# Optimization experiments

Measured on AMD Instinct MI355X. Metric: run time of the kernel, lower is better.

Reference implementation:

```python
import jax, jax.numpy as jnp
import numpy as np

K = 32                      # nsample (neighbors)
NPTS = [4096, 2048, 1024]   # npts // downsample_ratios [1,2,4]
CH = [(6, 64, 64), (134, 128, 128), (262, 256, 256)]  # (c_in_edge, c_mid, c_out) per EdgeConv
OUT_CH = 128
EPS = 1e-5


def setup_inputs():
    key = jax.random.key(0)
    ks = iter(jax.random.split(key, 64))
    d = {"pcd": jax.random.normal(next(ks), (8, 4096, 3), dtype=jnp.float32)}
    for li, (cin, cmid, cout) in enumerate(CH, start=1):
        d[f"W{li}a"] = jax.random.normal(next(ks), (cmid, cin), dtype=jnp.float32) * 0.05
        d[f"b{li}a"] = jax.random.normal(next(ks), (cmid,), dtype=jnp.float32) * 0.01
        d[f"g{li}a"] = jnp.ones((cmid,), dtype=jnp.float32)
        d[f"be{li}a"] = jnp.zeros((cmid,), dtype=jnp.float32)
        d[f"W{li}b"] = jax.random.normal(next(ks), (cout, cmid), dtype=jnp.float32) * 0.05
        d[f"b{li}b"] = jax.random.normal(next(ks), (cout,), dtype=jnp.float32) * 0.01
        d[f"g{li}b"] = jnp.ones((cout,), dtype=jnp.float32)
        d[f"be{li}b"] = jnp.zeros((cout,), dtype=jnp.float32)
    d["fcW"] = jax.random.normal(next(ks), (OUT_CH, CH[-1][2]), dtype=jnp.float32) * 0.05
    d["fcb"] = jnp.zeros((OUT_CH,), dtype=jnp.float32)
    return d


def _knn_idx(q, p, k):
    # q: [B,m,3] queries, p: [B,n,3] points -> [B,m,k] nearest-neighbor indices
    d = (jnp.sum(q * q, -1)[:, :, None] + jnp.sum(p * p, -1)[:, None, :]
         - 2.0 * jnp.einsum('bmd,bnd->bmn', q, p))
    _, idx = jax.lax.top_k(-d, k)
    return idx


def _bn(x, g, b):
    # training-mode BatchNorm2d over [B,C,m,k], biased variance (torch behavior)
    mu = jnp.mean(x, axis=(0, 2, 3), keepdims=True)
    var = jnp.mean((x - mu) ** 2, axis=(0, 2, 3), keepdims=True)
    return (x - mu) * jax.lax.rsqrt(var + EPS) * g[None, :, None, None] + b[None, :, None, None]


def _edge_conv(xyz, feat, npoints, params):
    # xyz: [B,n,3], feat: [B,C,n] or None. Range sampling = first npoints points.
    W1, b1, g1, be1, W2, b2, g2, be2 = params
    new_xyz = xyz[:, :npoints]
    # use_xyz=True: concat features (as [B,n,C]) with xyz
    f = xyz if feat is None else jnp.concatenate([jnp.transpose(feat, (0, 2, 1)), xyz], -1)
    new_f = f[:, :npoints]                       # [B,m,D]
    idx = _knn_idx(new_xyz, xyz, K)              # [B,m,K]
    knn_f = jax.vmap(lambda a, i: a[i])(f, idx)  # [B,m,K,D] gather
    tiled = jnp.broadcast_to(new_f[:, :, None, :], knn_f.shape)
    e = jnp.concatenate([knn_f - tiled, tiled], -1)  # [B,m,K,2D] edge features
    h = jnp.einsum('bmkc,oc->bomk', e, W1) + b1[None, :, None, None]
    h = jax.nn.relu(_bn(h, g1, be1))
    h = jnp.einsum('bcmk,oc->bomk', h, W2) + b2[None, :, None, None]
    h = jax.nn.relu(_bn(h, g2, be2))
    return new_xyz, jnp.max(h, axis=-1)          # max-pool over K -> [B,C,m]


def reference(pcd, W1a, b1a, g1a, be1a, W1b, b1b, g1b, be1b,
              W2a, b2a, g2a, be2a, W2b, b2b, g2b, be2b,
              W3a, b3a, g3a, be3a, W3b, b3b, g3b, be3b, fcW, fcb):
    xyz = pcd[..., :3]
    feat = None  # pcd has only xyz channels
    layer_params = [
        (W1a, b1a, g1a, be1a, W1b, b1b, g1b, be1b),
        (W2a, b2a, g2a, be2a, W2b, b2b, g2b, be2b),
        (W3a, b3a, g3a, be3a, W3b, b3b, g3b, be3b),
    ]
    for npoints, p in zip(NPTS, layer_params):
        xyz, feat = _edge_conv(xyz, feat, npoints, p)
    out_feat = jnp.einsum('bcn,oc->bon', feat, fcW) + fcb[None, :, None]
    # Range sampling: idx chain of aranges composes to arange(NPTS[-1])
    idx = jnp.broadcast_to(jnp.arange(NPTS[-1]), (pcd.shape[0], NPTS[-1]))
    return xyz, out_feat, idx, feat
```

## Files before the change

kernel.cpp:

```cpp
#include <hip/hip_runtime.h>
#include <hip/hip_bf16.h>

#define B8 8
#define KNN 32
typedef unsigned short u16;
typedef unsigned int u32;
typedef unsigned long long u64;

typedef __attribute__((ext_vector_type(8))) _Float16 half8;
typedef __attribute__((ext_vector_type(4))) float f32x4;

static __device__ __forceinline__ u16 f2h_u(float f) {
  _Float16 h = (_Float16)f; u16 u; __builtin_memcpy(&u, &h, 2); return u;
}

static __device__ __forceinline__ u64 enc_key(float d, int id) {
  u32 u = __float_as_uint(d);
  u = (d >= 0.f) ? (u | 0x80000000u) : ~u;
  return ((u64)u << 32) | (u32)id;
}
static __device__ __forceinline__ float dec_val(u64 k) {
  u32 u = (u32)(k >> 32);
  u = (u & 0x80000000u) ? (u & 0x7fffffffu) : ~u;
  return __uint_as_float(u);
}

static __device__ __forceinline__ u64 rank64(u64 mk, int lane, u64* slk, u64* outk, float& tau) {
  slk[lane] = mk;
  int r = 0;
#pragma unroll 16
  for (int j = 0; j < 64; ++j) r += (slk[j] < mk) ? 1 : 0;
  outk[r] = mk;
  u64 res = outk[lane];
  tau = dec_val(outk[31]);
  return res;
}

__global__ __launch_bounds__(256) void knn_kernel(const float* __restrict__ pcd,
                                                  int N, int M, int* __restrict__ idxout) {
  __shared__ float4 pts[1024];
  __shared__ u64 bufk[4][32];
  __shared__ u64 slk[4][64];
  __shared__ u64 outk[4][64];
  const int t = threadIdx.x;
  const int lane = t & 63, w = t >> 6;
  const int b = blockIdx.y;
  const int m = blockIdx.x * 4 + w;
  const float* base = pcd + (size_t)b * 4096 * 3;
  const float qx = base[m*3], qy = base[m*3+1], qz = base[m*3+2];
  const float ax = -2.f*qx, ay = -2.f*qy, az = -2.f*qz;

  u64 heldk; float tau; int cnt = 0;

  for (int i = t; i < 1024; i += 256) {
    const float* p = base + (size_t)i * 3;
    float x = p[0], y = p[1], z = p[2];
    pts[i] = make_float4(x, y, z, x*x + y*y + z*z);
  }
  __syncthreads();

  {
    float4 p = pts[lane];
    float r0 = fmaf(ax, p.x, fmaf(ay, p.y, fmaf(az, p.z, p.w)));
    heldk = rank64(enc_key(r0, lane), lane, slk[w], outk[w], tau);
  }

  for (int n0 = 0; n0 < N; n0 += 1024) {
    if (n0) {
      __syncthreads();
      for (int i = t; i < 1024; i += 256) {
        const float* p = base + (size_t)(n0 + i) * 3;
        float x = p[0], y = p[1], z = p[2];
        pts[i] = make_float4(x, y, z, x*x + y*y + z*z);
      }
      __syncthreads();
    }
    for (int c = 0; c < 1024; c += 256) {
      float4 p0 = pts[c + lane];
      float4 p1 = pts[c + 64 + lane];
      float4 p2 = pts[c + 128 + lane];
      float4 p3 = pts[c + 192 + lane];
      float r[4];
      r[0] = fmaf(ax, p0.x, fmaf(ay, p0.y, fmaf(az, p0.z, p0.w)));
      r[1] = fmaf(ax, p1.x, fmaf(ay, p1.y, fmaf(az, p1.z, p1.w)));
      r[2] = fmaf(ax, p2.x, fmaf(ay, p2.y, fmaf(az, p2.z, p2.w)));
      r[3] = fmaf(ax, p3.x, fmaf(ay, p3.y, fmaf(az, p3.z, p3.w)));
      if (n0 == 0 && c == 0) r[0] = 3.4e38f;
      float rmn = fminf(fminf(r[0], r[1]), fminf(r[2], r[3]));
      if (!__any(rmn < tau)) continue;
#pragma unroll
      for (int j = 0; j < 4; ++j) {
        float rr = r[j];
        if (!__any(rr < tau)) continue;
        int gid = n0 + c + j * 64 + lane;
        bool pass = rr < tau;
        while (__any(pass)) {
          u64 mk_ = __ballot(pass);
          int before = __popcll(mk_ & ((1ull << lane) - 1ull));
          int total  = __popcll(mk_);
          int room = 32 - cnt;
          if (pass && before < room) {
            bufk[w][cnt + before] = enc_key(rr, gid);
            pass = false;
          }
          if (total >= room) {
            u64 mk = (lane < 32) ? heldk : bufk[w][lane - 32];
            heldk = rank64(mk, lane, slk[w], outk[w], tau);
            cnt = 0;
            pass = pass && (rr < tau);
          } else {
            cnt += total;
          }
        }
      }
    }
  }
  if (cnt > 0) {
    int bl = lane - 32;
    u64 mk = (lane < 32) ? heldk
             : ((bl < cnt) ? bufk[w][bl]
                           : ((0xFFFFFFFFull << 32) | (0xFFFFFF00u | (u32)lane)));
    heldk = rank64(mk, lane, slk[w], outk[w], tau);
  }
  if (lane < KNN) idxout[((size_t)b * M + m) * KNN + lane] = (int)(u32)(heldk & 0xFFFFFFFFu);
}

__global__ void prep_all(
    const float* __restrict__ W1a, const float* __restrict__ W1b,
    const float* __restrict__ W2a, const float* __restrict__ W2b,
    const float* __restrict__ W3a, const float* __restrict__ W3b,
    float* __restrict__ RED,
    float* __restrict__ WAT1, float* __restrict__ WBT1, u16* __restrict__ WBH1,
    float* __restrict__ WBT2, u16* __restrict__ WAH2, u16* __restrict__ WBH2,
    float* __restrict__ WBT3, u16* __restrict__ WAH3, u16* __restrict__ WBH3)
{
  int i0 = blockIdx.x * 256 + threadIdx.x;
  int NT = gridDim.x * 256;
  for (int i = i0; i < 8192; i += NT) RED[i] = 0.f;
  for (int i = i0; i < 256; i += NT) {
    int c = i >> 6, o = i & 63;
    float w1 = (c < 3) ? W1a[o*6 + c] : 0.f;
    float w2 = (c < 3) ? W1a[o*6 + 3 + c] : 0.f;
    WAT1[i] = w1; WBT1[i] = w2 - w1;
  }
  for (int i = i0; i < 4096; i += NT) WBH1[i] = f2h_u(W1b[i]);
  for (int i = i0; i < 68*128; i += NT) {
    int c = i >> 7, o = i & 127;
    float w1 = 0.f, w2 = 0.f;
    if (c < 67) { w1 = W2a[o*134 + c]; w2 = W2a[o*134 + 67 + c]; }
    WBT2[i] = w2 - w1;
  }
  for (int i = i0; i < 128*128; i += NT) {
    int o = i >> 7, k = i & 127;
    WAH2[i] = (k < 67) ? f2h_u(W2a[o*134 + k]) : (u16)0;
  }
  for (int i = i0; i < 16384; i += NT) WBH2[i] = f2h_u(W2b[i]);
  for (int i = i0; i < 132*256; i += NT) {
    int c = i >> 8, o = i & 255;
    float w1 = 0.f, w2 = 0.f;
    if (c < 131) { w1 = W3a[o*262 + c]; w2 = W3a[o*262 + 131 + c]; }
    WBT3[i] = w2 - w1;
  }
  for (int i = i0; i < 256*192; i += NT) {
    int o = i / 192, k = i - o * 192;
    WAH3[i] = (k < 131) ? f2h_u(W3a[o*262 + k]) : (u16)0;
  }
  for (int i = i0; i < 65536; i += NT) WBH3[i] = f2h_u(W3b[i]);
}

template<int C2, int CM, int MODE>
__global__ __launch_bounds__(256) void conv_a_gemm(
    const float* __restrict__ F, size_t fbstride,
    const int* __restrict__ idx,
    const float* __restrict__ Wt,
    const float* __restrict__ bias,
    const float* __restrict__ T,
    float* __restrict__ Tout,
    float* __restrict__ red_s, float* __restrict__ red_q,
    int M)
{
  constexpr int KP = (C2 + 3) & ~3;
  constexpr int KC = (KP <= 68) ? KP : 44;
  __shared__ float At[64][KC];
  __shared__ float Wts[KC][64];
  __shared__ int ji[64];
  __shared__ float sred[4][64];
  __shared__ float qred[4][64];
  const int t = threadIdx.x;
  const int rt = blockIdx.x, ot = blockIdx.y, b = blockIdx.z;
  const int R0 = rt * 64, oc0 = ot * 64;
  const float* Fb = F + (size_t)b * fbstride;

  if (t < 64) {
    int gr = R0 + t;
    ji[t] = (MODE == 0) ? gr : idx[((size_t)b * M + (gr >> 5)) * KNN + (gr & 31)];
  }

  const int cg = t & 15, rg = t >> 4;
  const int r0 = rg * 4, c0 = cg * 4;
  float acc[4][4];
  if (MODE == 0) {
#pragma unroll
    for (int j = 0; j < 4; ++j) {
      float bv = bias[oc0 + c0 + j];
#pragma unroll
      for (int i = 0; i < 4; ++i) acc[i][j] = bv;
    }
  } else {
#pragma unroll
    for (int i = 0; i < 4; ++i) {
      const float* tp = T + ((size_t)b * M + (size_t)((R0 + r0 + i) >> 5)) * CM + oc0 + c0;
      acc[i][0] = tp[0]; acc[i][1] = tp[1]; acc[i][2] = tp[2]; acc[i][3] = tp[3];
    }
  }
  __syncthreads();

  for (int k0 = 0; k0 < KP; k0 += KC) {
    if (k0) __syncthreads();
    for (int i = t; i < KC * 64; i += 256) {
      int c = i >> 6, o = i & 63;
      Wts[c][o] = Wt[(size_t)(k0 + c) * CM + oc0 + o];
    }
    if constexpr (C2 == 3) {
      for (int i = t; i < 64 * 4; i += 256) {
        int r = i >> 2, c = i & 3;
        At[r][c] = (c < 3) ? Fb[(size_t)ji[r] * 3 + c] : 0.f;
      }
    } else {
      constexpr int C4 = KC / 4;
      for (int i = t; i < 64 * C4; i += 256) {
        int r = i / C4, c4 = i - r * C4;
        *(float4*)&At[r][c4 * 4] = *(const float4*)&Fb[(size_t)ji[r] * KP + k0 + c4 * 4];
      }
    }
    __syncthreads();

#pragma unroll 4
    for (int k = 0; k < KC; ++k) {
      const float4 w4 = *(const float4*)&Wts[k][c0];
      float a0 = At[r0][k], a1 = At[r0+1][k], a2 = At[r0+2][k], a3 = At[r0+3][k];
      acc[0][0]=fmaf(a0,w4.x,acc[0][0]); acc[0][1]=fmaf(a0,w4.y,acc[0][1]);
      acc[0][2]=fmaf(a0,w4.z,acc[0][2]); acc[0][3]=fmaf(a0,w4.w,acc[0][3]);
      acc[1][0]=fmaf(a1,w4.x,acc[1][0]); acc[1][1]=fmaf(a1,w4.y,acc[1][1]);
      acc[1][2]=fmaf(a1,w4.z,acc[1][2]); acc[1][3]=fmaf(a1,w4.w,acc[1][3]);
      acc[2][0]=fmaf(a2,w4.x,acc[2][0]); acc[2][1]=fmaf(a2,w4.y,acc[2][1]);
      acc[2][2]=fmaf(a2,w4.z,acc[2][2]); acc[2][3]=fmaf(a2,w4.w,acc[2][3]);
      acc[3][0]=fmaf(a3,w4.x,acc[3][0]); acc[3][1]=fmaf(a3,w4.y,acc[3][1]);
      acc[3][2]=fmaf(a3,w4.z,acc[3][2]); acc[3][3]=fmaf(a3,w4.w,acc[3][3]);
    }
  }

  if (MODE == 0) {
    float* op = Tout + ((size_t)b * M + R0) * (size_t)CM + oc0;
#pragma unroll
    for (int i = 0; i < 4; ++i) {
      float* p = op + (size_t)(r0 + i) * CM + c0;
      p[0]=acc[i][0]; p[1]=acc[i][1]; p[2]=acc[i][2]; p[3]=acc[i][3];
    }
  } else {
    float cs[4], cq_[4];
#pragma unroll
    for (int j = 0; j < 4; ++j) {
      float s = acc[0][j] + acc[1][j] + acc[2][j] + acc[3][j];
      float q = acc[0][j]*acc[0][j] + acc[1][j]*acc[1][j] + acc[2][j]*acc[2][j] + acc[3][j]*acc[3][j];
      s += __shfl_xor(s, 16); q += __shfl_xor(q, 16);
      s += __shfl_xor(s, 32); q += __shfl_xor(q, 32);
      cs[j] = s; cq_[j] = q;
    }
    const int wv = t >> 6;
    if ((t & 48) == 0) {
#pragma unroll
      for (int j = 0; j < 4; ++j) { sred[wv][c0 + j] = cs[j]; qred[wv][c0 + j] = cq_[j]; }
    }
    __syncthreads();
    if (t < 64) {
      float s = sred[0][t] + sred[1][t] + sred[2][t] + sred[3][t];
      float q = qred[0][t] + qred[1][t] + qred[2][t] + qred[3][t];
      int shdw = (rt & 15) * 256;
      atomicAdd(&red_s[shdw + t], s);
      atomicAdd(&red_q[shdw + t], q);
    }
  }
}

__global__ __launch_bounds__(256) void l1_convb(
    const float* __restrict__ pcd,
    const int* __restrict__ idx,
    const float* __restrict__ WAT,
    const float* __restrict__ T,
    const u16* __restrict__ Wbh,
    const float* __restrict__ bb,
    const float* __restrict__ sc1, const float* __restrict__ sh1,
    float* __restrict__ red_s, float* __restrict__ red_q,
    float* __restrict__ hmax)
{
  __shared__ u16 Alds[64][72];
  __shared__ u16 Wlds[64][72];
  __shared__ float xyzs[64][4];
  __shared__ float was[3][64];
  __shared__ float scs[64], shs[64];
  __shared__ int ji[64];
  const int t = threadIdx.x;
  const int lane = t & 63, w = t >> 6;
  const int wr = w >> 1, wc = w & 1;
  const int cl = lane & 15, rq = lane >> 4;
  const int rt = blockIdx.x, b = blockIdx.y;
  const int R0 = rt * 64;
  const float* pb = pcd + (size_t)b * 12288;

  if (t < 64) ji[t] = idx[((size_t)b * 4096 + ((R0 + t) >> 5)) * KNN + ((R0 + t) & 31)];
  if (t < 192) was[t / 64][t & 63] = WAT[t];
  for (int i = t; i < 64 * 8; i += 256) {
    int o = i >> 3, seg = i & 7;
    *(float4*)&Wlds[o][seg * 8] = *(const float4*)&Wbh[(size_t)o * 64 + seg * 8];
  }
  __syncthreads();
  if (t < 64) {
    const float* p = pb + (size_t)ji[t] * 3;
    xyzs[t][0] = p[0]; xyzs[t][1] = p[1]; xyzs[t][2] = p[2]; xyzs[t][3] = 0.f;
  }
  if (t < 64) { scs[t] = sc1[t]; shs[t] = sh1[t]; }
  __syncthreads();

  for (int i = t; i < 64 * 8; i += 256) {
    int r = i >> 3, seg = i & 7;
    float px = xyzs[r][0], py = xyzs[r][1], pz = xyzs[r][2];
    const float* Tm = T + ((size_t)b * 4096 + (size_t)((R0 + r) >> 5)) * 64;
    half8 ov;
#pragma unroll
    for (int j2 = 0; j2 < 8; ++j2) {
      int c = seg * 8 + j2;
      float h = Tm[c];
      h = fmaf(px, was[0][c], h);
      h = fmaf(py, was[1][c], h);
      h = fmaf(pz, was[2][c], h);
      ov[j2] = (_Float16)fmaxf(0.f, fmaf(h, scs[c], shs[c]));
    }
    *(half8*)&Alds[r][seg * 8] = ov;
  }
  __syncthreads();

  f32x4 acc[2][2];
#pragma unroll
  for (int fr = 0; fr < 2; ++fr)
#pragma unroll
    for (int fc = 0; fc < 2; ++fc) {
      float bv = bb[wc * 32 + fc * 16 + cl];
#pragma unroll
      for (int r = 0; r < 4; ++r) acc[fr][fc][r] = bv;
    }

#pragma unroll
  for (int kk = 0; kk < 2; ++kk) {
    half8 af[2], bf[2];
#pragma unroll
    for (int fr = 0; fr < 2; ++fr)
      af[fr] = *(const half8*)&Alds[wr*32 + fr*16 + cl][kk*32 + rq*8];
#pragma unroll
    for (int fc = 0; fc < 2; ++fc)
      bf[fc] = *(const half8*)&Wlds[wc*32 + fc*16 + cl][kk*32 + rq*8];
#pragma unroll
    for (int fr = 0; fr < 2; ++fr)
#pragma unroll
      for (int fc = 0; fc < 2; ++fc)
        acc[fr][fc] = __builtin_amdgcn_mfma_f32_16x16x32_f16(af[fr], bf[fc], acc[fr][fc], 0, 0, 0);
  }

#pragma unroll
  for (int fc = 0; fc < 2; ++fc) {
    float s = 0.f, q = 0.f, mx = -3.4e38f;
#pragma unroll
    for (int fr = 0; fr < 2; ++fr)
#pragma unroll
      for (int r = 0; r < 4; ++r) {
        float v = acc[fr][fc][r];
        s += v; q += v * v; mx = fmaxf(mx, v);
      }
    s += __shfl_xor(s, 16); q += __shfl_xor(q, 16); mx = fmaxf(mx, __shfl_xor(mx, 16));
    s += __shfl_xor(s, 32); q += __shfl_xor(q, 32); mx = fmaxf(mx, __shfl_xor(mx, 32));
    if (rq == 0) {
      int col = wc * 32 + fc * 16 + cl;
      int shdw = (rt & 15) * 256;
      atomicAdd(&red_s[shdw + col], s);
      atomicAdd(&red_q[shdw + col], q);
      hmax[((size_t)b * 4096 + (size_t)(rt * 2 + wr)) * 64 + col] = mx;
    }
  }
}

template<int CM, int KPAD>
__global__ __launch_bounds__(256) void conv_a_mfma(
    const float* __restrict__ F, int fstride, size_t fbstride,
    const int* __restrict__ idx,
    const u16* __restrict__ Wh,
    const float* __restrict__ T,
    u32* __restrict__ H32,
    float* __restrict__ red_s, float* __restrict__ red_q,
    int M)
{
  constexpr int FC = CM / 32;
  __shared__ u16 Alds[64][72];
  __shared__ u16 Wlds[CM][72];
  __shared__ int ji[64];
  const int t = threadIdx.x;
  const int lane = t & 63, w = t >> 6;
  const int wr = w >> 1, wc = w & 1;
  const int cl = lane & 15, rq = lane >> 4;
  const int rt = blockIdx.x, b = blockIdx.y;
  const int R0 = rt * 64;
  const float* Fb = F + (size_t)b * fbstride;

  if (t < 64) ji[t] = idx[((size_t)b * M + ((R0 + t) >> 5)) * KNN + ((R0 + t) & 31)];

  f32x4 acc[2][FC];
#pragma unroll
  for (int fr = 0; fr < 2; ++fr)
#pragma unroll
    for (int fc = 0; fc < FC; ++fc) {
      int col = wc * (CM/2) + fc * 16 + cl;
#pragma unroll
      for (int r = 0; r < 4; ++r) {
        int row = R0 + wr*32 + fr*16 + rq*4 + r;
        acc[fr][fc][r] = T[((size_t)b * M + (row >> 5)) * CM + col];
      }
    }
  __syncthreads();

  for (int k0 = 0; k0 < KPAD; k0 += 64) {
    if (k0) __syncthreads();
    for (int i = t; i < 64 * 16; i += 256) {
      int r = i >> 4, seg = i & 15;
      int k = k0 + seg * 4;
      ushort4 s = {0,0,0,0};
      if (k < fstride) {
        float4 v = *(const float4*)&Fb[(size_t)ji[r] * fstride + k];
        s.x = f2h_u(v.x); s.y = f2h_u(v.y); s.z = f2h_u(v.z); s.w = f2h_u(v.w);
      }
      *(ushort4*)&Alds[r][seg * 4] = s;
    }
    for (int i = t; i < CM * 8; i += 256) {
      int o = i >> 3, seg = i & 7;
      *(float4*)&Wlds[o][seg * 8] = *(const float4*)&Wh[(size_t)o * KPAD + k0 + seg * 8];
    }
    __syncthreads();

#pragma unroll
    for (int kk = 0; kk < 2; ++kk) {
      half8 af[2], bf[FC];
#pragma unroll
      for (int fr = 0; fr < 2; ++fr)
        af[fr] = *(const half8*)&Alds[wr*32 + fr*16 + cl][kk*32 + rq*8];
#pragma unroll
      for (int fc = 0; fc < FC; ++fc)
        bf[fc] = *(const half8*)&Wlds[wc*(CM/2) + fc*16 + cl][kk*32 + rq*8];
#pragma unroll
      for (int fr = 0; fr < 2; ++fr)
#pragma unroll
        for (int fc = 0; fc < FC; ++fc)
          acc[fr][fc] = __builtin_amdgcn_mfma_f32_16x16x32_f16(af[fr], bf[fc], acc[fr][fc], 0, 0, 0);
    }
  }

  u32* Hb4 = H32 + ((size_t)b * ((size_t)M * KNN / 4) + (size_t)(R0 >> 2)) * CM;
#pragma unroll
  for (int fr = 0; fr < 2; ++fr)
#pragma unroll
    for (int fc = 0; fc < FC; ++fc) {
      int col = wc*(CM/2) + fc*16 + cl;
      u32 v = __builtin_amdgcn_cvt_pk_fp8_f32(acc[fr][fc][0], acc[fr][fc][1], 0, false);
      v = __builtin_amdgcn_cvt_pk_fp8_f32(acc[fr][fc][2], acc[fr][fc][3], v, true);
      Hb4[(size_t)(wr*8 + fr*4 + rq) * CM + col] = v;
    }

#pragma unroll
  for (int fc = 0; fc < FC; ++fc) {
    float s = 0.f, q = 0.f;
#pragma unroll
    for (int fr = 0; fr < 2; ++fr)
#pragma unroll
      for (int r = 0; r < 4; ++r) {
        float v = acc[fr][fc][r];
        s += v; q += v * v;
      }
    s += __shfl_xor(s, 16); q += __shfl_xor(q, 16);
    s += __shfl_xor(s, 32); q += __shfl_xor(q, 32);
    if (rq == 0) {
      int col = wc*(CM/2) + fc*16 + cl;
      int shdw = (rt & 15) * 256;
      atomicAdd(&red_s[shdw + col], s);
      atomicAdd(&red_q[shdw + col], q);
    }
  }
}

template<int CM>
__global__ __launch_bounds__(512) void conv_b_fused(
    const u32* __restrict__ H32,
    const u16* __restrict__ Wh,
    const float* __restrict__ bb,
    const float* __restrict__ sc1, const float* __restrict__ sh1,
    float* __restrict__ red_s, float* __restrict__ red_q,
    float* __restrict__ hmax,
    int Mrows)
{
  constexpr int FC = CM / 32;
  __shared__ u16 Alds[128][72];
  __shared__ u16 Wlds[CM][72];
  __shared__ float scs[CM], shs[CM];
  const int t = threadIdx.x;
  const int lane = t & 63, w = t >> 6;
  const int wr = w >> 1;
  const int wc = w & 1;
  const int cl = lane & 15, rq = lane >> 4;
  const int rt = blockIdx.x, b = blockIdx.y;
  const u32* Hb4 = H32 + ((size_t)b * ((size_t)Mrows / 4) + (size_t)(rt * 32)) * CM;

  for (int i = t; i < CM; i += 512) { scs[i] = sc1[i]; shs[i] = sh1[i]; }

  f32x4 acc[2][FC];
#pragma unroll
  for (int fr = 0; fr < 2; ++fr)
#pragma unroll
    for (int fc = 0; fc < FC; ++fc) {
      float bv = bb[wc * (CM/2) + fc * 16 + cl];
#pragma unroll
      for (int r = 0; r < 4; ++r) acc[fr][fc][r] = bv;
    }
  __syncthreads();

  for (int k0 = 0; k0 < CM; k0 += 64) {
    if (k0) __syncthreads();
    for (int i = t; i < 128 * 8; i += 512) {
      int r = i >> 3, seg = i & 7;
      int rg = r >> 2, sh8 = (r & 3) * 8;
      const u32* hp = Hb4 + (size_t)rg * CM + k0 + seg * 8;
      half8 ov;
#pragma unroll
      for (int j = 0; j < 8; ++j) {
        float v = __builtin_amdgcn_cvt_f32_fp8((hp[j] >> sh8) & 0xffu, 0);
        int c = k0 + seg * 8 + j;
        v = fmaxf(0.f, fmaf(v, scs[c], shs[c]));
        ov[j] = (_Float16)v;
      }
      *(half8*)&Alds[r][seg * 8] = ov;
    }
    for (int i = t; i < CM * 8; i += 512) {
      int o = i >> 3, seg = i & 7;
      *(float4*)&Wlds[o][seg * 8] = *(const float4*)&Wh[(size_t)o * CM + k0 + seg * 8];
    }
    __syncthreads();

#pragma unroll
    for (int kk = 0; kk < 2; ++kk) {
      half8 af[2], bf[FC];
#pragma unroll
      for (int fr = 0; fr < 2; ++fr)
        af[fr] = *(const half8*)&Alds[wr*32 + fr*16 + cl][kk*32 + rq*8];
#pragma unroll
      for (int fc = 0; fc < FC; ++fc)
        bf[fc] = *(const half8*)&Wlds[wc*(CM/2) + fc*16 + cl][kk*32 + rq*8];
#pragma unroll
      for (int fr = 0; fr < 2; ++fr)
#pragma unroll
        for (int fc = 0; fc < FC; ++fc)
          acc[fr][fc] = __builtin_amdgcn_mfma_f32_16x16x32_f16(af[fr], bf[fc], acc[fr][fc], 0, 0, 0);
    }
  }

#pragma unroll
  for (int fc = 0; fc < FC; ++fc) {
    float s = 0.f, q = 0.f, mx = -3.4e38f;
#pragma unroll
    for (int fr = 0; fr < 2; ++fr)
#pragma unroll
      for (int r = 0; r < 4; ++r) {
        float v = acc[fr][fc][r];
        s += v; q += v * v; mx = fmaxf(mx, v);
      }
    s += __shfl_xor(s, 16); q += __shfl_xor(q, 16); mx = fmaxf(mx, __shfl_xor(mx, 16));
    s += __shfl_xor(s, 32); q += __shfl_xor(q, 32); mx = fmaxf(mx, __shfl_xor(mx, 32));
    if (rq == 0) {
      int col = wc*(CM/2) + fc*16 + cl;
      int shdw = (rt & 15) * 256;
      atomicAdd(&red_s[shdw + col], s);
      atomicAdd(&red_q[shdw + col], q);
      hmax[((size_t)b * (Mrows >> 5) + (size_t)(rt * 4 + wr)) * CM + col] = mx;
    }
  }
}

__global__ void bn_finalize(float* __restrict__ red_s, float* __restrict__ red_q,
                            const float* __restrict__ g, const float* __restrict__ be,
                            float* __restrict__ sc, float* __restrict__ sh,
                            int cm, float invcnt) {
  int o = threadIdx.x;
  if (o < cm) {
    float s = 0.f, q = 0.f;
    for (int i = 0; i < 16; ++i) { s += red_s[i * 256 + o]; q += red_q[i * 256 + o]; }
    float mu  = s * invcnt;
    float var = fmaxf(q * invcnt - mu * mu, 0.f);
    float scv = g[o] * rsqrtf(var + 1e-5f);
    sc[o] = scv;
    sh[o] = fmaf(-mu, scv, be[o]);
  }
  __syncthreads();
  for (int i = threadIdx.x; i < 16 * 256; i += 256) { red_s[i] = 0.f; red_q[i] = 0.f; }
}

__global__ __launch_bounds__(256) void bnrelu_fb(const float* __restrict__ hm,
    const float* __restrict__ sc2, const float* __restrict__ sh2,
    float* __restrict__ fout, int CM, int fostride, size_t fobstride, int M) {
  int i = blockIdx.x * 256 + threadIdx.x;
  int cq = CM >> 2;
  int total = B8 * M * cq;
  if (i >= total) return;
  int c4 = i % cq; int r = i / cq;
  int b = r / M, m = r - b * M;
  float4 v = *(const float4*)&hm[((size_t)b * M + m) * CM + c4 * 4];
  int c = c4 * 4;
  float4 o;
  o.x = fmaxf(0.f, fmaf(v.x, sc2[c],   sh2[c]));
  o.y = fmaxf(0.f, fmaf(v.y, sc2[c+1], sh2[c+1]));
  o.z = fmaxf(0.f, fmaf(v.z, sc2[c+2], sh2[c+2]));
  o.w = fmaxf(0.f, fmaf(v.w, sc2[c+3], sh2[c+3]));
  *(float4*)&fout[(size_t)b * fobstride + (size_t)m * fostride + c] = o;
}

__global__ void append_xyz(const float* __restrict__ pcd, float* __restrict__ fbuf,
                           int nrows, int stride, int coff) {
  int i = blockIdx.x * 256 + threadIdx.x;
  if (i < B8 * nrows) {
    int b = i / nrows, n = i - b * nrows;
    const float* p = pcd + ((size_t)b * 4096 + n) * 3;
    float* dd = fbuf + ((size_t)b * nrows + n) * stride + coff;
    dd[0] = p[0]; dd[1] = p[1]; dd[2] = p[2]; dd[3] = 0.f;
  }
}

__global__ __launch_bounds__(256) void fc_out(const float* __restrict__ f4,
                                              const float* __restrict__ fcW, const float* __restrict__ fcb,
                                              float* __restrict__ out1, float* __restrict__ out3) {
  __shared__ float tile[32 * 257];
  const int t = threadIdx.x, b = blockIdx.x, n0 = blockIdx.y * 32;
  for (int i = t; i < 32 * 256; i += 256) {
    int n = i >> 8, c = i & 255;
    tile[n * 257 + c] = f4[((size_t)b * 1024 + n0 + n) * 256 + c];
  }
  __syncthreads();
  const int n = t & 31, og = t >> 5;
#pragma unroll
  for (int ci = 0; ci < 32; ++ci) {
    int c = og * 32 + ci;
    out3[((size_t)b * 256 + c) * 1024 + n0 + n] = tile[n * 257 + c];
  }
#pragma unroll
  for (int oi = 0; oi < 16; ++oi) {
    int o = og * 16 + oi;
    float acc = fcb[o];
    const float* w = fcW + (size_t)o * 256;
#pragma unroll 4
    for (int c = 0; c < 256; ++c) acc = fmaf(tile[n * 257 + c], w[c], acc);
    out1[((size_t)b * 128 + o) * 1024 + n0 + n] = acc;
  }
}

__global__ void out_xyz_idx(const float* __restrict__ pcd, float* __restrict__ out0,
                            float* __restrict__ out2) {
  int i = blockIdx.x * 256 + threadIdx.x;
  if (i < B8 * 1024) {
    int b = i >> 10, n = i & 1023;
    const float* p = pcd + ((size_t)b * 4096 + n) * 3;
    float* o = out0 + (size_t)i * 3;
    o[0] = p[0]; o[1] = p[1]; o[2] = p[2];
    out2[i] = (float)n;
  }
}

extern "C" void kernel_launch(void* const* d_in, const int* in_sizes, int n_in,
                              void* d_out, int out_size, void* d_ws, size_t ws_size,
                              hipStream_t stream) {
  (void)in_sizes; (void)n_in; (void)out_size; (void)ws_size;
  const float* pcd = (const float*)d_in[0];
  const float* W1a = (const float*)d_in[1];  const float* b1a = (const float*)d_in[2];
  const float* g1a = (const float*)d_in[3];  const float* be1a= (const float*)d_in[4];
  const float* W1b = (const float*)d_in[5];  const float* b1b = (const float*)d_in[6];
  const float* g1b = (const float*)d_in[7];  const float* be1b= (const float*)d_in[8];
  const float* W2a = (const float*)d_in[9];  const float* b2a = (const float*)d_in[10];
  const float* g2a = (const float*)d_in[11]; const float* be2a= (const float*)d_in[12];
  const float* W2b = (const float*)d_in[13]; const float* b2b = (const float*)d_in[14];
  const float* g2b = (const float*)d_in[15]; const float* be2b= (const float*)d_in[16];
  const float* W3a = (const float*)d_in[17]; const float* b3a = (const float*)d_in[18];
  const float* g3a = (const float*)d_in[19]; const float* be3a= (const float*)d_in[20];
  const float* W3b = (const float*)d_in[21]; const float* b3b = (const float*)d_in[22];
  const float* g3b = (const float*)d_in[23]; const float* be3b= (const float*)d_in[24];
  const float* fcW = (const float*)d_in[25]; const float* fcb = (const float*)d_in[26];

  float* wsf = (float*)d_ws;
  float* FB2 = wsf;
  float* FB3 = FB2 + 2228224;
  float* FB4 = FB3 + 2162688;
  float* TBUF= FB4 + 2097152;
  float* RED = TBUF + 2097152;
  float* red_s = RED, *red_q = RED + 4096;
  float* SC1 = RED + 8192;  float* SH1 = SC1 + 256;
  float* SC2 = SH1 + 256;   float* SH2 = SC2 + 256;
  float* WAT1 = SH2 + 256;
  float* WBT1 = WAT1 + 256;
  float* WBT2 = WBT1 + 256;
  float* WBT3 = WBT2 + 8704;
  float* HMAX = WBT3 + 33792;
  int* IDX1 = (int*)(HMAX + 2097152);
  int* IDX2 = IDX1 + (size_t)8 * 4096 * 32;
  int* IDX3 = IDX2 + (size_t)8 * 2048 * 32;
  u32* H32  = (u32*)(IDX3 + (size_t)8 * 1024 * 32);
  u16* WBH1 = (u16*)(H32 + 16777216);
  u16* WAH2 = WBH1 + 4096;
  u16* WBH2 = WAH2 + 16384;
  u16* WAH3 = WBH2 + 16384;
  u16* WBH3 = WAH3 + 49152;

  float* out0 = (float*)d_out;
  float* out1 = out0 + 24576;
  float* out2 = out1 + 1048576;
  float* out3 = out2 + 8192;

  prep_all<<<64, 256, 0, stream>>>(W1a, W1b, W2a, W2b, W3a, W3b, RED,
                                   WAT1, WBT1, WBH1, WBT2, WAH2, WBH2, WBT3, WAH3, WBH3);

  knn_kernel<<<dim3(1024, 8), 256, 0, stream>>>(pcd, 4096, 4096, IDX1);
  conv_a_gemm<3,64,0><<<dim3(64,1,8),256,0,stream>>>(pcd,(size_t)12288,nullptr,WBT1,b1a,nullptr,TBUF,nullptr,nullptr,4096);
  conv_a_gemm<3,64,1><<<dim3(2048,1,8),256,0,stream>>>(pcd,(size_t)12288,IDX1,WAT1,nullptr,TBUF,nullptr,red_s,red_q,4096);
  bn_finalize<<<1,256,0,stream>>>(red_s,red_q,g1a,be1a,SC1,SH1,64,1.f/1048576.f);
  l1_convb<<<dim3(2048,8),256,0,stream>>>(pcd,IDX1,WAT1,TBUF,WBH1,b1b,SC1,SH1,red_s,red_q,HMAX);
  bn_finalize<<<1,256,0,stream>>>(red_s,red_q,g1b,be1b,SC2,SH2,64,1.f/1048576.f);
  bnrelu_fb<<<2048,256,0,stream>>>(HMAX,SC2,SH2,FB2,64,68,(size_t)278528,4096);
  append_xyz<<<128, 256, 0, stream>>>(pcd, FB2, 4096, 68, 64);

  knn_kernel<<<dim3(512, 8), 256, 0, stream>>>(pcd, 4096, 2048, IDX2);
  conv_a_gemm<67,128,0><<<dim3(32,2,8),256,0,stream>>>(FB2,(size_t)278528,nullptr,WBT2,b2a,nullptr,TBUF,nullptr,nullptr,2048);
  conv_a_mfma<128,128><<<dim3(1024,8),256,0,stream>>>(FB2,68,(size_t)278528,IDX2,WAH2,TBUF,H32,red_s,red_q,2048);
  bn_finalize<<<1,256,0,stream>>>(red_s,red_q,g2a,be2a,SC1,SH1,128,1.f/524288.f);
  conv_b_fused<128><<<dim3(512,8),512,0,stream>>>(H32,WBH2,b2b,SC1,SH1,red_s,red_q,HMAX,2048*32);
  bn_finalize<<<1,256,0,stream>>>(red_s,red_q,g2b,be2b,SC2,SH2,128,1.f/524288.f);
  bnrelu_fb<<<2048,256,0,stream>>>(HMAX,SC2,SH2,FB3,128,132,(size_t)270336,2048);
  append_xyz<<<64, 256, 0, stream>>>(pcd, FB3, 2048, 132, 128);

  knn_kernel<<<dim3(256, 8), 256, 0, stream>>>(pcd, 2048, 1024, IDX3);
  conv_a_gemm<131,256,0><<<dim3(16,4,8),256,0,stream>>>(FB3,(size_t)270336,nullptr,WBT3,b3a,nullptr,TBUF,nullptr,nullptr,1024);
  conv_a_mfma<256,192><<<dim3(512,8),256,0,stream>>>(FB3,132,(size_t)270336,IDX3,WAH3,TBUF,H32,red_s,red_q,1024);
  bn_finalize<<<1,256,0,stream>>>(red_s,red_q,g3a,be3a,SC1,SH1,256,1.f/262144.f);
  conv_b_fused<256><<<dim3(256,8),512,0,stream>>>(H32,WBH3,b3b,SC1,SH1,red_s,red_q,HMAX,1024*32);
  bn_finalize<<<1,256,0,stream>>>(red_s,red_q,g3b,be3b,SC2,SH2,256,1.f/262144.f);
  bnrelu_fb<<<2048,256,0,stream>>>(HMAX,SC2,SH2,FB4,256,256,(size_t)262144,1024);

  fc_out<<<dim3(8, 32), 256, 0, stream>>>(FB4, fcW, fcb, out1, out3);
  out_xyz_idx<<<32, 256, 0, stream>>>(pcd, out0, out2);
}
```

Before: 849.7 us.

## Reuse layer-1 kNN indices for layer 2 and vectorize kNN point loads

Layer 2 queries the first 2048 points against the same 4096-point cloud that layer 1 already searched, so its neighbor lists are identical to the first rows of IDX1. The second kNN launch is removed, and conv_a_mfma gains an index-stride parameter so it can read IDX1 directly. Separately, the kNN kernel now stages points into shared memory with three float4 loads per thread instead of scalar strided loads. The reuse depends on layer-2 sampling being exactly the first points of the same xyz set.

```diff
diff --git a/kernel.cpp b/kernel.cpp
--- a/kernel.cpp
+++ b/kernel.cpp
@@ -52,10 +52,13 @@
 
   u64 heldk; float tau; int cnt = 0;
 
-  for (int i = t; i < 1024; i += 256) {
-    const float* p = base + (size_t)i * 3;
-    float x = p[0], y = p[1], z = p[2];
-    pts[i] = make_float4(x, y, z, x*x + y*y + z*z);
+  {
+    const float4* src = (const float4*)(base) + (size_t)t * 3;
+    float4 va = src[0], vb = src[1], vc = src[2];
+    pts[t*4+0] = make_float4(va.x, va.y, va.z, fmaf(va.x,va.x, fmaf(va.y,va.y, va.z*va.z)));
+    pts[t*4+1] = make_float4(va.w, vb.x, vb.y, fmaf(va.w,va.w, fmaf(vb.x,vb.x, vb.y*vb.y)));
+    pts[t*4+2] = make_float4(vb.z, vb.w, vc.x, fmaf(vb.z,vb.z, fmaf(vb.w,vb.w, vc.x*vc.x)));
+    pts[t*4+3] = make_float4(vc.y, vc.z, vc.w, fmaf(vc.y,vc.y, fmaf(vc.z,vc.z, vc.w*vc.w)));
   }
   __syncthreads();
 
@@ -68,11 +71,12 @@
   for (int n0 = 0; n0 < N; n0 += 1024) {
     if (n0) {
       __syncthreads();
-      for (int i = t; i < 1024; i += 256) {
-        const float* p = base + (size_t)(n0 + i) * 3;
-        float x = p[0], y = p[1], z = p[2];
-        pts[i] = make_float4(x, y, z, x*x + y*y + z*z);
-      }
+      const float4* src = (const float4*)(base + (size_t)n0 * 3) + (size_t)t * 3;
+      float4 va = src[0], vb = src[1], vc = src[2];
+      pts[t*4+0] = make_float4(va.x, va.y, va.z, fmaf(va.x,va.x, fmaf(va.y,va.y, va.z*va.z)));
+      pts[t*4+1] = make_float4(va.w, vb.x, vb.y, fmaf(va.w,va.w, fmaf(vb.x,vb.x, vb.y*vb.y)));
+      pts[t*4+2] = make_float4(vb.z, vb.w, vc.x, fmaf(vb.z,vb.z, fmaf(vb.w,vb.w, vc.x*vc.x)));
+      pts[t*4+3] = make_float4(vc.y, vc.z, vc.w, fmaf(vc.y,vc.y, fmaf(vc.z,vc.z, vc.w*vc.w)));
       __syncthreads();
     }
     for (int c = 0; c < 1024; c += 256) {
@@ -391,7 +395,7 @@
 template<int CM, int KPAD>
 __global__ __launch_bounds__(256) void conv_a_mfma(
     const float* __restrict__ F, int fstride, size_t fbstride,
-    const int* __restrict__ idx,
+    const int* __restrict__ idx, int idxstride,
     const u16* __restrict__ Wh,
     const float* __restrict__ T,
     u32* __restrict__ H32,
@@ -410,7 +414,7 @@
   const int R0 = rt * 64;
   const float* Fb = F + (size_t)b * fbstride;
 
-  if (t < 64) ji[t] = idx[((size_t)b * M + ((R0 + t) >> 5)) * KNN + ((R0 + t) & 31)];
+  if (t < 64) ji[t] = idx[((size_t)b * idxstride + ((R0 + t) >> 5)) * KNN + ((R0 + t) & 31)];
 
   f32x4 acc[2][FC];
 #pragma unroll
@@ -710,8 +714,7 @@
   float* WBT3 = WBT2 + 8704;
   float* HMAX = WBT3 + 33792;
   int* IDX1 = (int*)(HMAX + 2097152);
-  int* IDX2 = IDX1 + (size_t)8 * 4096 * 32;
-  int* IDX3 = IDX2 + (size_t)8 * 2048 * 32;
+  int* IDX3 = IDX1 + (size_t)8 * 4096 * 32;
   u32* H32  = (u32*)(IDX3 + (size_t)8 * 1024 * 32);
   u16* WBH1 = (u16*)(H32 + 16777216);
   u16* WAH2 = WBH1 + 4096;
@@ -736,9 +739,8 @@
   bnrelu_fb<<<2048,256,0,stream>>>(HMAX,SC2,SH2,FB2,64,68,(size_t)278528,4096);
   append_xyz<<<128, 256, 0, stream>>>(pcd, FB2, 4096, 68, 64);
 
-  knn_kernel<<<dim3(512, 8), 256, 0, stream>>>(pcd, 4096, 2048, IDX2);
   conv_a_gemm<67,128,0><<<dim3(32,2,8),256,0,stream>>>(FB2,(size_t)278528,nullptr,WBT2,b2a,nullptr,TBUF,nullptr,nullptr,2048);
-  conv_a_mfma<128,128><<<dim3(1024,8),256,0,stream>>>(FB2,68,(size_t)278528,IDX2,WAH2,TBUF,H32,red_s,red_q,2048);
+  conv_a_mfma<128,128><<<dim3(1024,8),256,0,stream>>>(FB2,68,(size_t)278528,IDX1,4096,WAH2,TBUF,H32,red_s,red_q,2048);
   bn_finalize<<<1,256,0,stream>>>(red_s,red_q,g2a,be2a,SC1,SH1,128,1.f/524288.f);
   conv_b_fused<128><<<dim3(512,8),512,0,stream>>>(H32,WBH2,b2b,SC1,SH1,red_s,red_q,HMAX,2048*32);
   bn_finalize<<<1,256,0,stream>>>(red_s,red_q,g2b,be2b,SC2,SH2,128,1.f/524288.f);
@@ -747,7 +749,7 @@
 
   knn_kernel<<<dim3(256, 8), 256, 0, stream>>>(pcd, 2048, 1024, IDX3);
   conv_a_gemm<131,256,0><<<dim3(16,4,8),256,0,stream>>>(FB3,(size_t)270336,nullptr,WBT3,b3a,nullptr,TBUF,nullptr,nullptr,1024);
-  conv_a_mfma<256,192><<<dim3(512,8),256,0,stream>>>(FB3,132,(size_t)270336,IDX3,WAH3,TBUF,H32,red_s,red_q,1024);
+  conv_a_mfma<256,192><<<dim3(512,8),256,0,stream>>>(FB3,132,(size_t)270336,IDX3,1024,WAH3,TBUF,H32,red_s,red_q,1024);
   bn_finalize<<<1,256,0,stream>>>(red_s,red_q,g3a,be3a,SC1,SH1,256,1.f/262144.f);
   conv_b_fused<256><<<dim3(256,8),512,0,stream>>>(H32,WBH3,b3b,SC1,SH1,red_s,red_q,HMAX,1024*32);
   bn_finalize<<<1,256,0,stream>>>(red_s,red_q,g3b,be3b,SC2,SH2,256,1.f/262144.f);
```

After: 774.1 us. 8.9% less time.

## Split KNN queries across wave pairs, fuse BN finalize, reuse layer-1 KNN

Applied to the files above, without the earlier changes.

The KNN kernel now gives each query two wavefronts, each scanning half of the point tile and sharing their pruning threshold, then merges the two partial top-32 lists. This doubles the grid to raise parallelism on the dominant KNN stage. The separate bn_finalize launches are removed: each consumer kernel computes scale and shift from per-layer reduction buffers, which are zeroed once in prep. The append_xyz kernel is folded into bnrelu_fb. Layer 2 reuses IDX1, because the first 2048 points' neighbours among all 4096 points are the same as layer 1's, so the second KNN launch is dropped. The cost is some redundant per-block BN arithmetic and extra sync and merge work in KNN.

```diff
diff --git a/kernel.cpp b/kernel.cpp
--- a/kernel.cpp
+++ b/kernel.cpp
@@ -36,17 +36,33 @@
   return res;
 }
 
+static __device__ __forceinline__ void bn_from_red(int o, const float* red_s, const float* red_q,
+                                                   const float* g, const float* be, float invcnt,
+                                                   float* scs, float* shs) {
+  float s = 0.f, q = 0.f;
+#pragma unroll
+  for (int i = 0; i < 16; ++i) { s += red_s[i * 256 + o]; q += red_q[i * 256 + o]; }
+  float mu  = s * invcnt;
+  float var = fmaxf(q * invcnt - mu * mu, 0.f);
+  float scv = g[o] * rsqrtf(var + 1e-5f);
+  scs[o] = scv;
+  shs[o] = fmaf(-mu, scv, be[o]);
+}
+
 __global__ __launch_bounds__(256) void knn_kernel(const float* __restrict__ pcd,
                                                   int N, int M, int* __restrict__ idxout) {
   __shared__ float4 pts[1024];
   __shared__ u64 bufk[4][32];
   __shared__ u64 slk[4][64];
   __shared__ u64 outk[4][64];
+  __shared__ float taus[4];
+  __shared__ u64 mergek[2][32];
   const int t = threadIdx.x;
   const int lane = t & 63, w = t >> 6;
+  const int q = w >> 1, h = w & 1;
   const int b = blockIdx.y;
-  const int m = blockIdx.x * 4 + w;
-  const float* base = pcd + (size_t)b * 4096 * 3;
+  const int m = blockIdx.x * 2 + q;
+  const float* base = pcd + (size_t)b * 12288;
   const float qx = base[m*3], qy = base[m*3+1], qz = base[m*3+2];
   const float ax = -2.f*qx, ay = -2.f*qy, az = -2.f*qz;
 
@@ -60,13 +76,14 @@
   __syncthreads();
 
   {
-    float4 p = pts[lane];
+    float4 p = pts[h * 512 + lane];
     float r0 = fmaf(ax, p.x, fmaf(ay, p.y, fmaf(az, p.z, p.w)));
-    heldk = rank64(enc_key(r0, lane), lane, slk[w], outk[w], tau);
+    heldk = rank64(enc_key(r0, h * 512 + lane), lane, slk[w], outk[w], tau);
   }
 
   for (int n0 = 0; n0 < N; n0 += 1024) {
     if (n0) {
+      taus[w] = tau;
       __syncthreads();
       for (int i = t; i < 1024; i += 256) {
         const float* p = base + (size_t)(n0 + i) * 3;
@@ -74,8 +91,10 @@
         pts[i] = make_float4(x, y, z, x*x + y*y + z*z);
       }
       __syncthreads();
-    }
-    for (int c = 0; c < 1024; c += 256) {
+      tau = fminf(tau, taus[w ^ 1]);
+    }
+    for (int cc = 0; cc < 512; cc += 256) {
+      const int c = h * 512 + cc;
       float4 p0 = pts[c + lane];
       float4 p1 = pts[c + 64 + lane];
       float4 p2 = pts[c + 128 + lane];
@@ -85,7 +104,7 @@
       r[1] = fmaf(ax, p1.x, fmaf(ay, p1.y, fmaf(az, p1.z, p1.w)));
       r[2] = fmaf(ax, p2.x, fmaf(ay, p2.y, fmaf(az, p2.z, p2.w)));
       r[3] = fmaf(ax, p3.x, fmaf(ay, p3.y, fmaf(az, p3.z, p3.w)));
-      if (n0 == 0 && c == 0) r[0] = 3.4e38f;
+      if (n0 == 0 && cc == 0) r[0] = 3.4e38f;
       float rmn = fminf(fminf(r[0], r[1]), fminf(r[2], r[3]));
       if (!__any(rmn < tau)) continue;
 #pragma unroll
@@ -122,7 +141,13 @@
                            : ((0xFFFFFFFFull << 32) | (0xFFFFFF00u | (u32)lane)));
     heldk = rank64(mk, lane, slk[w], outk[w], tau);
   }
-  if (lane < KNN) idxout[((size_t)b * M + m) * KNN + lane] = (int)(u32)(heldk & 0xFFFFFFFFu);
+  if (h == 1 && lane < 32) mergek[q][lane] = heldk;
+  __syncthreads();
+  if (h == 0) {
+    u64 mk = (lane < 32) ? heldk : mergek[q][lane - 32];
+    heldk = rank64(mk, lane, slk[w], outk[w], tau);
+    if (lane < 32) idxout[((size_t)b * M + m) * KNN + lane] = (int)(u32)(heldk & 0xFFFFFFFFu);
+  }
 }
 
 __global__ void prep_all(
@@ -136,7 +161,7 @@
 {
   int i0 = blockIdx.x * 256 + threadIdx.x;
   int NT = gridDim.x * 256;
-  for (int i = i0; i < 8192; i += NT) RED[i] = 0.f;
+  for (int i = i0; i < 49152; i += NT) RED[i] = 0.f;
   for (int i = i0; i < 256; i += NT) {
     int c = i >> 6, o = i & 63;
     float w1 = (c < 3) ? W1a[o*6 + c] : 0.f;
@@ -290,8 +315,9 @@
     const float* __restrict__ T,
     const u16* __restrict__ Wbh,
     const float* __restrict__ bb,
-    const float* __restrict__ sc1, const float* __restrict__ sh1,
-    float* __restrict__ red_s, float* __restrict__ red_q,
+    const float* __restrict__ gA, const float* __restrict__ beA,
+    const float* __restrict__ redA_s, const float* __restrict__ redA_q,
+    float* __restrict__ redB_s, float* __restrict__ redB_q,
     float* __restrict__ hmax)
 {
   __shared__ u16 Alds[64][72];
@@ -310,6 +336,7 @@
 
   if (t < 64) ji[t] = idx[((size_t)b * 4096 + ((R0 + t) >> 5)) * KNN + ((R0 + t) & 31)];
   if (t < 192) was[t / 64][t & 63] = WAT[t];
+  if (t >= 192) bn_from_red(t - 192, redA_s, redA_q, gA, beA, 1.f/1048576.f, scs, shs);
   for (int i = t; i < 64 * 8; i += 256) {
     int o = i >> 3, seg = i & 7;
     *(float4*)&Wlds[o][seg * 8] = *(const float4*)&Wbh[(size_t)o * 64 + seg * 8];
@@ -319,7 +346,6 @@
     const float* p = pb + (size_t)ji[t] * 3;
     xyzs[t][0] = p[0]; xyzs[t][1] = p[1]; xyzs[t][2] = p[2]; xyzs[t][3] = 0.f;
   }
-  if (t < 64) { scs[t] = sc1[t]; shs[t] = sh1[t]; }
   __syncthreads();
 
   for (int i = t; i < 64 * 8; i += 256) {
@@ -330,11 +356,11 @@
 #pragma unroll
     for (int j2 = 0; j2 < 8; ++j2) {
       int c = seg * 8 + j2;
-      float h = Tm[c];
-      h = fmaf(px, was[0][c], h);
-      h = fmaf(py, was[1][c], h);
-      h = fmaf(pz, was[2][c], h);
-      ov[j2] = (_Float16)fmaxf(0.f, fmaf(h, scs[c], shs[c]));
+      float hh = Tm[c];
+      hh = fmaf(px, was[0][c], hh);
+      hh = fmaf(py, was[1][c], hh);
+      hh = fmaf(pz, was[2][c], hh);
+      ov[j2] = (_Float16)fmaxf(0.f, fmaf(hh, scs[c], shs[c]));
     }
     *(half8*)&Alds[r][seg * 8] = ov;
   }
@@ -381,8 +407,8 @@
     if (rq == 0) {
       int col = wc * 32 + fc * 16 + cl;
       int shdw = (rt & 15) * 256;
-      atomicAdd(&red_s[shdw + col], s);
-      atomicAdd(&red_q[shdw + col], q);
+      atomicAdd(&redB_s[shdw + col], s);
+      atomicAdd(&redB_q[shdw + col], q);
       hmax[((size_t)b * 4096 + (size_t)(rt * 2 + wr)) * 64 + col] = mx;
     }
   }
@@ -391,7 +417,7 @@
 template<int CM, int KPAD>
 __global__ __launch_bounds__(256) void conv_a_mfma(
     const float* __restrict__ F, int fstride, size_t fbstride,
-    const int* __restrict__ idx,
+    const int* __restrict__ idx, int idxstride,
     const u16* __restrict__ Wh,
     const float* __restrict__ T,
     u32* __restrict__ H32,
@@ -410,7 +436,7 @@
   const int R0 = rt * 64;
   const float* Fb = F + (size_t)b * fbstride;
 
-  if (t < 64) ji[t] = idx[((size_t)b * M + ((R0 + t) >> 5)) * KNN + ((R0 + t) & 31)];
+  if (t < 64) ji[t] = idx[((size_t)b * idxstride + ((R0 + t) >> 5)) * KNN + ((R0 + t) & 31)];
 
   f32x4 acc[2][FC];
 #pragma unroll
@@ -498,8 +524,9 @@
     const u32* __restrict__ H32,
     const u16* __restrict__ Wh,
     const float* __restrict__ bb,
-    const float* __restrict__ sc1, const float* __restrict__ sh1,
-    float* __restrict__ red_s, float* __restrict__ red_q,
+    const float* __restrict__ gA, const float* __restrict__ beA,
+    const float* __restrict__ redA_s, const float* __restrict__ redA_q, float invcnt,
+    float* __restrict__ redB_s, float* __restrict__ redB_q,
     float* __restrict__ hmax,
     int Mrows)
 {
@@ -515,7 +542,7 @@
   const int rt = blockIdx.x, b = blockIdx.y;
   const u32* Hb4 = H32 + ((size_t)b * ((size_t)Mrows / 4) + (size_t)(rt * 32)) * CM;
 
-  for (int i = t; i < CM; i += 512) { scs[i] = sc1[i]; shs[i] = sh1[i]; }
+  for (int i = t; i < CM; i += 512) bn_from_red(i, redA_s, redA_q, gA, beA, invcnt, scs, shs);
 
   f32x4 acc[2][FC];
 #pragma unroll
@@ -582,34 +609,21 @@
     if (rq == 0) {
       int col = wc*(CM/2) + fc*16 + cl;
       int shdw = (rt & 15) * 256;
-      atomicAdd(&red_s[shdw + col], s);
-      atomicAdd(&red_q[shdw + col], q);
+      atomicAdd(&redB_s[shdw + col], s);
+      atomicAdd(&redB_q[shdw + col], q);
       hmax[((size_t)b * (Mrows >> 5) + (size_t)(rt * 4 + wr)) * CM + col] = mx;
     }
   }
 }
 
-__global__ void bn_finalize(float* __restrict__ red_s, float* __restrict__ red_q,
-                            const float* __restrict__ g, const float* __restrict__ be,
-                            float* __restrict__ sc, float* __restrict__ sh,
-                            int cm, float invcnt) {
-  int o = threadIdx.x;
-  if (o < cm) {
-    float s = 0.f, q = 0.f;
-    for (int i = 0; i < 16; ++i) { s += red_s[i * 256 + o]; q += red_q[i * 256 + o]; }
-    float mu  = s * invcnt;
-    float var = fmaxf(q * invcnt - mu * mu, 0.f);
-    float scv = g[o] * rsqrtf(var + 1e-5f);
-    sc[o] = scv;
-    sh[o] = fmaf(-mu, scv, be[o]);
-  }
-  __syncthreads();
-  for (int i = threadIdx.x; i < 16 * 256; i += 256) { red_s[i] = 0.f; red_q[i] = 0.f; }
-}
-
 __global__ __launch_bounds__(256) void bnrelu_fb(const float* __restrict__ hm,
-    const float* __restrict__ sc2, const float* __restrict__ sh2,
+    const float* __restrict__ gB, const float* __restrict__ beB,
+    const float* __restrict__ redB_s, const float* __restrict__ redB_q, float invcnt,
+    const float* __restrict__ pcd,
     float* __restrict__ fout, int CM, int fostride, size_t fobstride, int M) {
+  __shared__ float scs[256], shs[256];
+  for (int o = threadIdx.x; o < CM; o += 256) bn_from_red(o, redB_s, redB_q, gB, beB, invcnt, scs, shs);
+  __syncthreads();
   int i = blockIdx.x * 256 + threadIdx.x;
   int cq = CM >> 2;
   int total = B8 * M * cq;
@@ -619,21 +633,15 @@
   float4 v = *(const float4*)&hm[((size_t)b * M + m) * CM + c4 * 4];
   int c = c4 * 4;
   float4 o;
-  o.x = fmaxf(0.f, fmaf(v.x, sc2[c],   sh2[c]));
-  o.y = fmaxf(0.f, fmaf(v.y, sc2[c+1], sh2[c+1]));
-  o.z = fmaxf(0.f, fmaf(v.z, sc2[c+2], sh2[c+2]));
-  o.w = fmaxf(0.f, fmaf(v.w, sc2[c+3], sh2[c+3]));
-  *(float4*)&fout[(size_t)b * fobstride + (size_t)m * fostride + c] = o;
-}
-
-__global__ void append_xyz(const float* __restrict__ pcd, float* __restrict__ fbuf,
-                           int nrows, int stride, int coff) {
-  int i = blockIdx.x * 256 + threadIdx.x;
-  if (i < B8 * nrows) {
-    int b = i / nrows, n = i - b * nrows;
-    const float* p = pcd + ((size_t)b * 4096 + n) * 3;
-    float* dd = fbuf + ((size_t)b * nrows + n) * stride + coff;
-    dd[0] = p[0]; dd[1] = p[1]; dd[2] = p[2]; dd[3] = 0.f;
+  o.x = fmaxf(0.f, fmaf(v.x, scs[c],   shs[c]));
+  o.y = fmaxf(0.f, fmaf(v.y, scs[c+1], shs[c+1]));
+  o.z = fmaxf(0.f, fmaf(v.z, scs[c+2], shs[c+2]));
+  o.w = fmaxf(0.f, fmaf(v.w, scs[c+3], shs[c+3]));
+  float* op = fout + (size_t)b * fobstride + (size_t)m * fostride;
+  *(float4*)(op + c) = o;
+  if (pcd && c4 == 0) {
+    const float* p = pcd + ((size_t)b * 4096 + m) * 3;
+    *(float4*)(op + CM) = make_float4(p[0], p[1], p[2], 0.f);
   }
 }
 
@@ -701,17 +709,16 @@
   float* FB4 = FB3 + 2162688;
   float* TBUF= FB4 + 2097152;
   float* RED = TBUF + 2097152;
-  float* red_s = RED, *red_q = RED + 4096;
-  float* SC1 = RED + 8192;  float* SH1 = SC1 + 256;
-  float* SC2 = SH1 + 256;   float* SH2 = SC2 + 256;
-  float* WAT1 = SH2 + 256;
+  float* R1A = RED;          float* R1B = RED + 8192;
+  float* R2A = RED + 16384;  float* R2B = RED + 24576;
+  float* R3A = RED + 32768;  float* R3B = RED + 40960;
+  float* WAT1 = RED + 49152;
   float* WBT1 = WAT1 + 256;
   float* WBT2 = WBT1 + 256;
   float* WBT3 = WBT2 + 8704;
   float* HMAX = WBT3 + 33792;
   int* IDX1 = (int*)(HMAX + 2097152);
-  int* IDX2 = IDX1 + (size_t)8 * 4096 * 32;
-  int* IDX3 = IDX2 + (size_t)8 * 2048 * 32;
+  int* IDX3 = IDX1 + (size_t)8 * 4096 * 32;
   u32* H32  = (u32*)(IDX3 + (size_t)8 * 1024 * 32);
   u16* WBH1 = (u16*)(H32 + 16777216);
   u16* WAH2 = WBH1 + 4096;
@@ -727,31 +734,22 @@
   prep_all<<<64, 256, 0, stream>>>(W1a, W1b, W2a, W2b, W3a, W3b, RED,
                                    WAT1, WBT1, WBH1, WBT2, WAH2, WBH2, WBT3, WAH3, WBH3);
 
-  knn_kernel<<<dim3(1024, 8), 256, 0, stream>>>(pcd, 4096, 4096, IDX1);
+  knn_kernel<<<dim3(2048, 8), 256, 0, stream>>>(pcd, 4096, 4096, IDX1);
   conv_a_gemm<3,64,0><<<dim3(64,1,8),256,0,stream>>>(pcd,(size_t)12288,nullptr,WBT1,b1a,nullptr,TBUF,nullptr,nullptr,4096);
-  conv_a_gemm<3,64,1><<<dim3(2048,1,8),256,0,stream>>>(pcd,(size_t)12288,IDX1,WAT1,nullptr,TBUF,nullptr,red_s,red_q,4096);
-  bn_finalize<<<1,256,0,stream>>>(red_s,red_q,g1a,be1a,SC1,SH1,64,1.f/1048576.f);
-  l1_convb<<<dim3(2048,8),256,0,stream>>>(pcd,IDX1,WAT1,TBUF,WBH1,b1b,SC1,SH1,red_s,red_q,HMAX);
-  bn_finalize<<<1,256,0,stream>>>(red_s,red_q,g1b,be1b,SC2,SH2,64,1.f/1048576.f);
-  bnrelu_fb<<<2048,256,0,stream>>>(HMAX,SC2,SH2,FB2,64,68,(size_t)278528,4096);
-  append_xyz<<<128, 256, 0, stream>>>(pcd, FB2, 4096, 68, 64);
-
-  knn_kernel<<<dim3(512, 8), 256, 0, stream>>>(pcd, 4096, 2048, IDX2);
+  conv_a_gemm<3,64,1><<<dim3(2048,1,8),256,0,stream>>>(pcd,(size_t)12288,IDX1,WAT1,nullptr,TBUF,nullptr,R1A,R1A+4096,4096);
+  l1_convb<<<dim3(2048,8),256,0,stream>>>(pcd,IDX1,WAT1,TBUF,WBH1,b1b,g1a,be1a,R1A,R1A+4096,R1B,R1B+4096,HMAX);
+  bnrelu_fb<<<2048,256,0,stream>>>(HMAX,g1b,be1b,R1B,R1B+4096,1.f/1048576.f,pcd,FB2,64,68,(size_t)278528,4096);
+
   conv_a_gemm<67,128,0><<<dim3(32,2,8),256,0,stream>>>(FB2,(size_t)278528,nullptr,WBT2,b2a,nullptr,TBUF,nullptr,nullptr,2048);
-  conv_a_mfma<128,128><<<dim3(1024,8),256,0,stream>>>(FB2,68,(size_t)278528,IDX2,WAH2,TBUF,H32,red_s,red_q,2048);
-  bn_finalize<<<1,256,0,stream>>>(red_s,red_q,g2a,be2a,SC1,SH1,128,1.f/524288.f);
-  conv_b_fused<128><<<dim3(512,8),512,0,stream>>>(H32,WBH2,b2b,SC1,SH1,red_s,red_q,HMAX,2048*32);
-  bn_finalize<<<1,256,0,stream>>>(red_s,red_q,g2b,be2b,SC2,SH2,128,1.f/524288.f);
-  bnrelu_fb<<<2048,256,0,stream>>>(HMAX,SC2,SH2,FB3,128,132,(size_t)270336,2048);
-  append_xyz<<<64, 256, 0, stream>>>(pcd, FB3, 2048, 132, 128);
-
-  knn_kernel<<<dim3(256, 8), 256, 0, stream>>>(pcd, 2048, 1024, IDX3);
+  conv_a_mfma<128,128><<<dim3(1024,8),256,0,stream>>>(FB2,68,(size_t)278528,IDX1,4096,WAH2,TBUF,H32,R2A,R2A+4096,2048);
+  conv_b_fused<128><<<dim3(512,8),512,0,stream>>>(H32,WBH2,b2b,g2a,be2a,R2A,R2A+4096,1.f/524288.f,R2B,R2B+4096,HMAX,2048*32);
+  bnrelu_fb<<<2048,256,0,stream>>>(HMAX,g2b,be2b,R2B,R2B+4096,1.f/524288.f,pcd,FB3,128,132,(size_t)270336,2048);
+
+  knn_kernel<<<dim3(512, 8), 256, 0, stream>>>(pcd, 2048, 1024, IDX3);
   conv_a_gemm<131,256,0><<<dim3(16,4,8),256,0,stream>>>(FB3,(size_t)270336,nullptr,WBT3,b3a,nullptr,TBUF,nullptr,nullptr,1024);
-  conv_a_mfma<256,192><<<dim3(512,8),256,0,stream>>>(FB3,132,(size_t)270336,IDX3,WAH3,TBUF,H32,red_s,red_q,1024);
-  bn_finalize<<<1,256,0,stream>>>(red_s,red_q,g3a,be3a,SC1,SH1,256,1.f/262144.f);
-  conv_b_fused<256><<<dim3(256,8),512,0,stream>>>(H32,WBH3,b3b,SC1,SH1,red_s,red_q,HMAX,1024*32);
-  bn_finalize<<<1,256,0,stream>>>(red_s,red_q,g3b,be3b,SC2,SH2,256,1.f/262144.f);
-  bnrelu_fb<<<2048,256,0,stream>>>(HMAX,SC2,SH2,FB4,256,256,(size_t)262144,1024);
+  conv_a_mfma<256,192><<<dim3(512,8),256,0,stream>>>(FB3,132,(size_t)270336,IDX3,1024,WAH3,TBUF,H32,R3A,R3A+4096,1024);
+  conv_b_fused<256><<<dim3(256,8),512,0,stream>>>(H32,WBH3,b3b,g3a,be3a,R3A,R3A+4096,1.f/262144.f,R3B,R3B+4096,HMAX,1024*32);
+  bnrelu_fb<<<2048,256,0,stream>>>(HMAX,g3b,be3b,R3B,R3B+4096,1.f/262144.f,nullptr,FB4,256,256,(size_t)262144,1024);
 
   fc_out<<<dim3(8, 32), 256, 0, stream>>>(FB4, fcW, fcb, out1, out3);
   out_xyz_idx<<<32, 256, 0, stream>>>(pcd, out0, out2);
```

Result: slower. 873.4 us (+2.8%).
